# Kernel tuning notes

Hardware: AMD Instinct MI355X
Metric: run time of the kernel (lower is better)

The kernel has to match this reference:

```python
import jax, jax.numpy as jnp
import numpy as np

E = 1024  # embed_dim
NH = 16   # num_heads
HH, WW = 128, 128


def setup_inputs() -> dict:
    key = jax.random.key(0)
    ks = jax.random.split(key, 9)
    s = 0.02
    x = jax.random.normal(ks[0], (1, HH, WW, E), dtype=jnp.float32)
    d = {"x": x}
    for i, name in enumerate(["q", "k", "v", "o"]):
        d[f"W{name}"] = jax.random.normal(ks[1 + 2 * i], (E, E), dtype=jnp.float32) * s
        d[f"b{name}"] = jax.random.normal(ks[2 + 2 * i], (E,), dtype=jnp.float32) * s
    return d


def reference(x, Wq, bq, Wk, bk, Wv, bv, Wo, bo):
    B, h, w, e = x.shape
    D = e // NH  # head dim
    # projections + ReLU feature map on q, k (torch Linear: x @ W.T + b)
    q = jnp.maximum(x @ Wq.T + bq, 0.0).reshape(B, h, w, NH, D)
    k = jnp.maximum(x @ Wk.T + bk, 0.0).reshape(B, h, w, NH, D)
    v = (x @ Wv.T + bv).reshape(B, h, w, NH, D)
    # width-axis linear retention: kv state per (row h, head n)
    kv_w = jnp.einsum('bhwnd,bhwne->bhnde', k, v)        # [B,h,NH,D,D]
    out = jnp.einsum('bhwnd,bhnde->bhwne', q, kv_w)      # [B,h,w,NH,D]
    # height-axis linear retention: kv state per (col w, head n)
    kv_h = jnp.einsum('bhwnd,bhwne->bwnde', k, v)        # [B,w,NH,D,D]
    out = jnp.einsum('bhwne,bwnef->bhwnf', out, kv_h)    # [B,h,w,NH,D]
    out = out.reshape(B, h, w, e) @ Wo.T + bo
    return out.reshape(B, h * w, e)
```

## Files before the change

kernel.cpp:

```cpp
#include <hip/hip_runtime.h>
#include <hip/hip_bf16.h>
#include <stdint.h>


typedef __attribute__((ext_vector_type(4))) float floatx4;
typedef __attribute__((ext_vector_type(8))) short shortx8;

static __device__ __forceinline__ float bf2f(unsigned short h) {
  return __uint_as_float(((unsigned int)h) << 16);
}
static __device__ __forceinline__ unsigned short f2bf(float f) {
  unsigned int u = __float_as_uint(f);
  u += 0x7fffu + ((u >> 16) & 1u);
  return (unsigned short)(u >> 16);
}

static __device__ __forceinline__ void gload16(const void* g, void* l) {
  __builtin_amdgcn_global_load_lds(
      (const __attribute__((address_space(1))) void*)g,
      (__attribute__((address_space(3))) void*)l, 16, 0, 0);
}

__global__ __launch_bounds__(256) void cvt_all(
    const float* __restrict__ x, const float* __restrict__ Wq,
    const float* __restrict__ Wk, const float* __restrict__ Wv,
    const float* __restrict__ Wo, unsigned short* __restrict__ xb,
    unsigned short* __restrict__ wqkvb, unsigned short* __restrict__ wob) {
  const int b = blockIdx.x;
  const float* src;
  unsigned short* dst;
  int off;
  if (b < 16384) {
    src = x; dst = xb; off = b;
  } else if (b < 17408) {
    src = Wq; dst = wqkvb; off = b - 16384;
  } else if (b < 18432) {
    src = Wk; dst = wqkvb + 1048576; off = b - 17408;
  } else if (b < 19456) {
    src = Wv; dst = wqkvb + 2097152; off = b - 18432;
  } else {
    src = Wo; dst = wob; off = b - 19456;
  }
  const int i = (off * 256 + threadIdx.x) * 4;
  float4 f = *(const float4*)(src + i);
  ushort4 o;
  o.x = f2bf(f.x); o.y = f2bf(f.y); o.z = f2bf(f.z); o.w = f2bf(f.w);
  *(ushort4*)(dst + i) = o;
}

template <int MODE>
__global__ __launch_bounds__(256) void gemm_bt(
    const unsigned short* __restrict__ A,
    const unsigned short* __restrict__ BT,
    const float* __restrict__ b0, const float* __restrict__ b1,
    const float* __restrict__ b2,
    unsigned short* __restrict__ Oq, unsigned short* __restrict__ Ok,
    unsigned short* __restrict__ Ov, float* __restrict__ Of) {
  __shared__ __align__(16) unsigned short smem[18432];
  unsigned short* lA = smem;
  unsigned short* lB = smem + 4096;
  const int K = 1024;
  const int t = threadIdx.x;
  const int m0 = blockIdx.x * 128;
  const int n0 = blockIdx.y * 128;
  const int lane = t & 63;
  const int wv = t >> 6;
  const int wm = (wv & 1) * 64;
  const int wn = (wv >> 1) * 64;
  const int mrow = lane & 15;
  const int quad = lane >> 4;
  const int slot = quad ^ ((mrow >> 1) & 3);

  const int srow = t >> 2;
  const int scol = (((t & 3) ^ ((srow >> 1) & 3))) * 8;
  const unsigned short* gA0 = A + (size_t)(m0 + srow) * K + scol;
  const unsigned short* gA1 = A + (size_t)(m0 + 64 + srow) * K + scol;
  const unsigned short* gB0 = BT + (size_t)(n0 + srow) * K + scol;
  const unsigned short* gB1 = BT + (size_t)(n0 + 64 + srow) * K + scol;
  unsigned short* lA0 = &lA[t * 8];
  unsigned short* lA1 = &lA[2048 + t * 8];
  unsigned short* lB0 = &lB[t * 8];
  unsigned short* lB1 = &lB[2048 + t * 8];

  floatx4 acc[4][4] = {};
  for (int kk = 0; kk < K; kk += 32) {
    gload16(gA0 + kk, lA0);
    gload16(gA1 + kk, lA1);
    gload16(gB0 + kk, lB0);
    gload16(gB1 + kk, lB1);
    __syncthreads();
    shortx8 af[4], bfr[4];
#pragma unroll
    for (int i = 0; i < 4; ++i)
      af[i] = *(const shortx8*)&lA[(wm + i * 16 + mrow) * 32 + slot * 8];
#pragma unroll
    for (int j = 0; j < 4; ++j)
      bfr[j] = *(const shortx8*)&lB[(wn + j * 16 + mrow) * 32 + slot * 8];
#pragma unroll
    for (int i = 0; i < 4; ++i)
#pragma unroll
      for (int j = 0; j < 4; ++j)
        acc[i][j] = __builtin_amdgcn_mfma_f32_16x16x32_bf16(af[i], bfr[j],
                                                            acc[i][j], 0, 0, 0);
    __syncthreads();
  }

  if (MODE == 0) {
    const int sel = n0 >> 10;
    const float* bb = (sel == 0) ? b0 : ((sel == 1) ? b1 : b2);
    unsigned short* O = (sel == 0) ? Oq : ((sel == 1) ? Ok : Ov);
    const int nb = n0 & 1023;
    unsigned short* we = smem + wv * 4608;
#pragma unroll
    for (int j = 0; j < 4; ++j) {
      const int coll = j * 16 + mrow;
      const float bias = bb[nb + wn + coll];
#pragma unroll
      for (int i = 0; i < 4; ++i) {
#pragma unroll
        for (int r = 0; r < 4; ++r) {
          const int rowl = i * 16 + quad * 4 + r;
          float v = acc[i][j][r] + bias;
          if (sel < 2) v = fmaxf(v, 0.0f);
          we[rowl * 72 + coll] = f2bf(v);
        }
      }
    }
    __syncthreads();
    const int r8 = lane >> 3;
    const int c8 = lane & 7;
#pragma unroll
    for (int p = 0; p < 8; ++p) {
      const int rowl = r8 + p * 8;
      uint4 v = *(const uint4*)&we[rowl * 72 + c8 * 8];
      *(uint4*)&O[(size_t)(m0 + wm + rowl) * 1024 + nb + wn + c8 * 8] = v;
    }
  } else {
    float* wef = (float*)smem;
    float* we = wef + (wv & 1) * (64 * 68);
    const int r8 = lane >> 3;
    const int c8 = lane & 7;
#pragma unroll
    for (int round = 0; round < 2; ++round) {
      if ((wv >> 1) == round) {
#pragma unroll
        for (int j = 0; j < 4; ++j) {
          const int coll = j * 16 + mrow;
          const float bias = b0[n0 + wn + coll];
#pragma unroll
          for (int i = 0; i < 4; ++i) {
#pragma unroll
            for (int r = 0; r < 4; ++r)
              we[(i * 16 + quad * 4 + r) * 68 + coll] = acc[i][j][r] + bias;
          }
        }
      }
      __syncthreads();
      if ((wv >> 1) == round) {
#pragma unroll
        for (int p = 0; p < 8; ++p) {
          const int rowl = r8 + p * 8;
          float4 v0 = *(const float4*)&we[rowl * 68 + c8 * 8];
          float4 v1 = *(const float4*)&we[rowl * 68 + c8 * 8 + 4];
          float* dst = Of + (size_t)(m0 + wm + rowl) * 1024 + n0 + wn + c8 * 8;
          *(float4*)dst = v0;
          *(float4*)(dst + 4) = v1;
        }
      }
      __syncthreads();
    }
  }
}

__global__ __launch_bounds__(256) void retention_fused(
    const unsigned short* __restrict__ S, const unsigned short* __restrict__ Kb,
    const unsigned short* __restrict__ Vb, unsigned short* __restrict__ D,
    int axis) {
  const int outer = blockIdx.x;
  const int n = blockIdx.y;
  __shared__ unsigned short lS[128 * 72];
  __shared__ unsigned short lKT[64 * 136];
  __shared__ unsigned short lVT[64 * 136];
  unsigned short* lKV = lVT;
  const int t = threadIdx.x;
  const size_t base = (axis == 0) ? ((size_t)outer << 17) : ((size_t)outer << 10);
  const size_t istr = (axis == 0) ? (size_t)1024 : (size_t)131072;
  const size_t nof = (size_t)(n << 6);

#pragma unroll
  for (int it = 0; it < 4; ++it) {
    const int r = it * 32 + (t >> 3);
    const int c = (t & 7) * 8;
    uint4 v = *(const uint4*)&S[base + (size_t)r * istr + nof + c];
    *(uint4*)&lS[r * 72 + c] = v;
  }
#pragma unroll
  for (int it = 0; it < 4; ++it) {
    const int w = it * 32 + (t & 31);
    const int d0 = (t >> 5) * 8;
    const size_t g = base + (size_t)w * istr + nof + d0;
    uint4 k4 = *(const uint4*)&Kb[g];
    uint4 v4 = *(const uint4*)&Vb[g];
    const unsigned short* kp = (const unsigned short*)&k4;
    const unsigned short* vp = (const unsigned short*)&v4;
#pragma unroll
    for (int i = 0; i < 8; ++i) {
      lKT[(d0 + i) * 136 + w] = kp[i];
      lVT[(d0 + i) * 136 + w] = vp[i];
    }
  }
  __syncthreads();

  const int lane = t & 63;
  const int wv = t >> 6;
  const int mrow = lane & 15;
  const int quad = lane >> 4;

  floatx4 acc1[4] = {};
#pragma unroll
  for (int ks = 0; ks < 4; ++ks) {
    shortx8 a = *(const shortx8*)&lVT[(wv * 16 + mrow) * 136 + ks * 32 + quad * 8];
#pragma unroll
    for (int j = 0; j < 4; ++j) {
      shortx8 b = *(const shortx8*)&lKT[(j * 16 + mrow) * 136 + ks * 32 + quad * 8];
      acc1[j] = __builtin_amdgcn_mfma_f32_16x16x32_bf16(a, b, acc1[j], 0, 0, 0);
    }
  }
  __syncthreads();
#pragma unroll
  for (int j = 0; j < 4; ++j)
#pragma unroll
    for (int r = 0; r < 4; ++r)
      lKV[(wv * 16 + quad * 4 + r) * 72 + j * 16 + mrow] = f2bf(acc1[j][r]);
  __syncthreads();

  floatx4 acc2[2][4] = {};
#pragma unroll
  for (int ks = 0; ks < 2; ++ks) {
    shortx8 a2[2], b2[4];
#pragma unroll
    for (int i = 0; i < 2; ++i)
      a2[i] = *(const shortx8*)&lS[(wv * 32 + i * 16 + mrow) * 72 + ks * 32 + quad * 8];
#pragma unroll
    for (int j = 0; j < 4; ++j)
      b2[j] = *(const shortx8*)&lKV[(j * 16 + mrow) * 72 + ks * 32 + quad * 8];
#pragma unroll
    for (int i = 0; i < 2; ++i)
#pragma unroll
      for (int j = 0; j < 4; ++j)
        acc2[i][j] = __builtin_amdgcn_mfma_f32_16x16x32_bf16(a2[i], b2[j],
                                                             acc2[i][j], 0, 0, 0);
  }
  __syncthreads();
#pragma unroll
  for (int i = 0; i < 2; ++i)
#pragma unroll
    for (int j = 0; j < 4; ++j)
#pragma unroll
      for (int r = 0; r < 4; ++r) {
        const int row = wv * 32 + i * 16 + quad * 4 + r;
        const int col = j * 16 + mrow;
        lS[row * 72 + col] = f2bf(acc2[i][j][r]);
      }
  __syncthreads();
#pragma unroll
  for (int it = 0; it < 4; ++it) {
    const int row = it * 32 + (t >> 3);
    const int c = (t & 7) * 8;
    uint4 v = *(const uint4*)&lS[row * 72 + c];
    *(uint4*)&D[base + (size_t)row * istr + nof + c] = v;
  }
}

extern "C" void kernel_launch(void* const* d_in, const int* in_sizes, int n_in,
                              void* d_out, int out_size, void* d_ws, size_t ws_size,
                              hipStream_t stream) {
  const float* x  = (const float*)d_in[0];
  const float* Wq = (const float*)d_in[1];
  const float* bq = (const float*)d_in[2];
  const float* Wk = (const float*)d_in[3];
  const float* bk = (const float*)d_in[4];
  const float* Wv = (const float*)d_in[5];
  const float* bv = (const float*)d_in[6];
  const float* Wo = (const float*)d_in[7];
  const float* bo = (const float*)d_in[8];
  float* out = (float*)d_out;

  char* ws = (char*)d_ws;
  unsigned short* xb    = (unsigned short*)(ws + 0);
  unsigned short* wqkvb = (unsigned short*)(ws + 33554432);
  unsigned short* wob   = (unsigned short*)(ws + 39845888);
  unsigned short* qb    = (unsigned short*)(ws + 41943040);
  unsigned short* kb    = (unsigned short*)(ws + 75497472);
  unsigned short* vb    = (unsigned short*)(ws + 109051904);
  unsigned short* out1  = xb;
  unsigned short* out2  = qb;

  cvt_all<<<dim3(20480), dim3(256), 0, stream>>>(x, Wq, Wk, Wv, Wo, xb, wqkvb, wob);
  gemm_bt<0><<<dim3(128, 24), dim3(256), 0, stream>>>(
      xb, wqkvb, bq, bk, bv, qb, kb, vb, (float*)nullptr);
  retention_fused<<<dim3(128, 16), dim3(256), 0, stream>>>(qb, kb, vb, out1, 0);
  retention_fused<<<dim3(128, 16), dim3(256), 0, stream>>>(out1, kb, vb, out2, 1);
  gemm_bt<1><<<dim3(128, 8), dim3(256), 0, stream>>>(
      out2, wob, bo, nullptr, nullptr, nullptr, nullptr, nullptr, out);
}
```

Before: 350.6 us.

## Replace 128x128 GEMM with double-buffered 256x256 tile, 8-wave pipelined kernel

The QKV and output projection GEMMs now use 256x256 tiles with 512 threads, K-step 64, and double-buffered LDS staging. Global-to-LDS loads for the next tiles are interleaved between MFMA quarter-blocks using explicit vmcnt waits, barriers and setprio. Block IDs are remapped so neighbouring blocks share A/B rows in cache, and the epilogue uses an XOR-swizzled LDS layout. The aim is to hide memory latency and raise data reuse per tile. In exchange the kernel uses 128KB of LDS and more registers, and the grid gets smaller (768 and 256 blocks).

```diff
diff --git a/kernel.cpp b/kernel.cpp
--- a/kernel.cpp
+++ b/kernel.cpp
@@ -6,9 +6,6 @@
 typedef __attribute__((ext_vector_type(4))) float floatx4;
 typedef __attribute__((ext_vector_type(8))) short shortx8;
 
-static __device__ __forceinline__ float bf2f(unsigned short h) {
-  return __uint_as_float(((unsigned int)h) << 16);
-}
 static __device__ __forceinline__ unsigned short f2bf(float f) {
   unsigned int u = __float_as_uint(f);
   u += 0x7fffu + ((u >> 16) & 1u);
@@ -48,61 +45,142 @@
   *(ushort4*)(dst + i) = o;
 }
 
+#define BARRIER()                           \
+  do {                                      \
+    asm volatile("" ::: "memory");          \
+    __builtin_amdgcn_s_barrier();           \
+    asm volatile("" ::: "memory");          \
+  } while (0)
+#define LGKM0 asm volatile("s_waitcnt lgkmcnt(0)" ::: "memory")
+#define VMCNT(N) asm volatile("s_waitcnt vmcnt(" #N ")" ::: "memory")
+
 template <int MODE>
-__global__ __launch_bounds__(256) void gemm_bt(
+__global__ __launch_bounds__(512, 2) void gemm256(
     const unsigned short* __restrict__ A,
     const unsigned short* __restrict__ BT,
     const float* __restrict__ b0, const float* __restrict__ b1,
     const float* __restrict__ b2,
     unsigned short* __restrict__ Oq, unsigned short* __restrict__ Ok,
     unsigned short* __restrict__ Ov, float* __restrict__ Of) {
-  __shared__ __align__(16) unsigned short smem[18432];
-  unsigned short* lA = smem;
-  unsigned short* lB = smem + 4096;
-  const int K = 1024;
+  __shared__ __align__(16) unsigned short smem[65536];
   const int t = threadIdx.x;
-  const int m0 = blockIdx.x * 128;
-  const int n0 = blockIdx.y * 128;
-  const int lane = t & 63;
-  const int wv = t >> 6;
-  const int wm = (wv & 1) * 64;
-  const int wn = (wv >> 1) * 64;
-  const int mrow = lane & 15;
-  const int quad = lane >> 4;
-  const int slot = quad ^ ((mrow >> 1) & 3);
-
-  const int srow = t >> 2;
-  const int scol = (((t & 3) ^ ((srow >> 1) & 3))) * 8;
-  const unsigned short* gA0 = A + (size_t)(m0 + srow) * K + scol;
-  const unsigned short* gA1 = A + (size_t)(m0 + 64 + srow) * K + scol;
-  const unsigned short* gB0 = BT + (size_t)(n0 + srow) * K + scol;
-  const unsigned short* gB1 = BT + (size_t)(n0 + 64 + srow) * K + scol;
-  unsigned short* lA0 = &lA[t * 8];
-  unsigned short* lA1 = &lA[2048 + t * 8];
-  unsigned short* lB0 = &lB[t * 8];
-  unsigned short* lB1 = &lB[2048 + t * 8];
-
-  floatx4 acc[4][4] = {};
-  for (int kk = 0; kk < K; kk += 32) {
-    gload16(gA0 + kk, lA0);
-    gload16(gA1 + kk, lA1);
-    gload16(gB0 + kk, lB0);
-    gload16(gB1 + kk, lB1);
-    __syncthreads();
-    shortx8 af[4], bfr[4];
-#pragma unroll
-    for (int i = 0; i < 4; ++i)
-      af[i] = *(const shortx8*)&lA[(wm + i * 16 + mrow) * 32 + slot * 8];
-#pragma unroll
-    for (int j = 0; j < 4; ++j)
-      bfr[j] = *(const shortx8*)&lB[(wn + j * 16 + mrow) * 32 + slot * 8];
-#pragma unroll
-    for (int i = 0; i < 4; ++i)
-#pragma unroll
-      for (int j = 0; j < 4; ++j)
-        acc[i][j] = __builtin_amdgcn_mfma_f32_16x16x32_bf16(af[i], bfr[j],
-                                                            acc[i][j], 0, 0, 0);
-    __syncthreads();
+  const int lane = t & 63, wid = t >> 6;
+  const int wm = wid >> 2, wn = wid & 3;
+  const int mrow = lane & 15, quad = lane >> 4;
+
+  int bid = blockIdx.x, bm, bn;
+  if (MODE == 0) {
+    int s = (bid & 7) * 96 + (bid >> 3);
+    bm = s / 12; bn = s - bm * 12;
+  } else {
+    int s = (bid & 7) * 32 + (bid >> 3);
+    bm = s >> 2; bn = s & 3;
+  }
+  const int m0 = bm << 8;
+  const int n0 = bn << 8;
+
+  const int sw0 = ((quad ^ (mrow & 7)) << 3);
+  const int sw1 = (((quad ^ 4) ^ (mrow & 7)) << 3);
+  const int a_base = wm * 8192 + mrow * 64;
+  const int b_base = 16384 + (wn >> 1) * 8192 + (((wn & 1) << 6) + mrow) * 64;
+  const int s_dst0 = wid * 512 + lane * 8;
+  const int srow = wid * 8 + (lane >> 3);
+  const int csrc = ((lane & 7) ^ (lane >> 3)) << 3;
+  const unsigned short* gAbase = A + (size_t)(m0 + srow) * 1024 + csrc;
+  const unsigned short* gBbase = BT + (size_t)(n0 + srow) * 1024 + csrc;
+
+#define STAGE_A(KT, H)                                              \
+  do {                                                              \
+    const unsigned short* _g = gAbase + ((H) << 17) + ((KT) << 6);  \
+    const int _d = (((KT) & 1) << 15) + ((H) << 13) + s_dst0;       \
+    gload16(_g, &smem[_d]);                                         \
+    gload16(_g + 65536, &smem[_d + 4096]);                          \
+  } while (0)
+#define STAGE_B(KT, H)                                                     \
+  do {                                                                     \
+    const unsigned short* _g = gBbase + ((H) << 17) + ((KT) << 6);         \
+    const int _d = (((KT) & 1) << 15) + 16384 + ((H) << 13) + s_dst0;      \
+    gload16(_g, &smem[_d]);                                                \
+    gload16(_g + 65536, &smem[_d + 4096]);                                 \
+  } while (0)
+#define LDA(MH)                                                  \
+  do {                                                           \
+    const int _ab = cb + a_base + ((MH) << 12);                  \
+    _Pragma("unroll") for (int i = 0; i < 4; ++i) {              \
+      aF[i][0] = *(const shortx8*)&smem[_ab + i * 1024 + sw0];   \
+      aF[i][1] = *(const shortx8*)&smem[_ab + i * 1024 + sw1];   \
+    }                                                            \
+  } while (0)
+#define LDB(NH)                                                      \
+  do {                                                               \
+    const int _bb = cb + b_base + ((NH) << 11);                      \
+    _Pragma("unroll") for (int j = 0; j < 2; ++j) {                  \
+      bF[NH][j][0] = *(const shortx8*)&smem[_bb + j * 1024 + sw0];   \
+      bF[NH][j][1] = *(const shortx8*)&smem[_bb + j * 1024 + sw1];   \
+    }                                                                \
+  } while (0)
+#define MFMAQ(MH, NH)                                                        \
+  do {                                                                       \
+    _Pragma("unroll") for (int ks = 0; ks < 2; ++ks)                         \
+    _Pragma("unroll") for (int i = 0; i < 4; ++i)                            \
+    _Pragma("unroll") for (int j = 0; j < 2; ++j)                            \
+      acc[(MH) * 4 + i][(NH) * 2 + j] =                                      \
+          __builtin_amdgcn_mfma_f32_16x16x32_bf16(                           \
+              aF[i][ks], bF[NH][j][ks], acc[(MH) * 4 + i][(NH) * 2 + j], 0,  \
+              0, 0);                                                         \
+  } while (0)
+
+  floatx4 acc[8][4] = {};
+  shortx8 aF[4][2];
+  shortx8 bF[2][2][2];
+
+  STAGE_A(0, 0); STAGE_A(0, 1);
+  STAGE_B(0, 0); STAGE_B(0, 1);
+  STAGE_B(1, 0); STAGE_B(1, 1);
+  VMCNT(4);
+  BARRIER();
+
+#pragma unroll 2
+  for (int kt = 0; kt < 16; ++kt) {
+    const int cb = (kt & 1) << 15;
+    LDA(0);
+    LDB(0);
+    if (kt < 15) STAGE_A(kt + 1, 0);
+    BARRIER();
+    LGKM0;
+    __builtin_amdgcn_sched_barrier(0);
+    __builtin_amdgcn_s_setprio(1);
+    MFMAQ(0, 0);
+    __builtin_amdgcn_s_setprio(0);
+    BARRIER();
+    LDB(1);
+    if (kt < 15) STAGE_A(kt + 1, 1);
+    BARRIER();
+    LGKM0;
+    __builtin_amdgcn_sched_barrier(0);
+    __builtin_amdgcn_s_setprio(1);
+    MFMAQ(0, 1);
+    __builtin_amdgcn_s_setprio(0);
+    BARRIER();
+    LDA(1);
+    if (kt < 14) STAGE_B(kt + 2, 0);
+    BARRIER();
+    LGKM0;
+    __builtin_amdgcn_sched_barrier(0);
+    __builtin_amdgcn_s_setprio(1);
+    MFMAQ(1, 1);
+    __builtin_amdgcn_s_setprio(0);
+    BARRIER();
+    if (kt < 14) STAGE_B(kt + 2, 1);
+    __builtin_amdgcn_s_setprio(1);
+    MFMAQ(1, 0);
+    __builtin_amdgcn_s_setprio(0);
+    if (kt < 14) {
+      VMCNT(4);
+    } else {
+      VMCNT(0);
+    }
+    BARRIER();
   }
 
   if (MODE == 0) {
@@ -110,66 +188,66 @@
     const float* bb = (sel == 0) ? b0 : ((sel == 1) ? b1 : b2);
     unsigned short* O = (sel == 0) ? Oq : ((sel == 1) ? Ok : Ov);
     const int nb = n0 & 1023;
-    unsigned short* we = smem + wv * 4608;
-#pragma unroll
-    for (int j = 0; j < 4; ++j) {
-      const int coll = j * 16 + mrow;
-      const float bias = bb[nb + wn + coll];
-#pragma unroll
-      for (int i = 0; i < 4; ++i) {
+    float bias[4];
+#pragma unroll
+    for (int j = 0; j < 4; ++j) bias[j] = bb[nb + wn * 64 + j * 16 + mrow];
+    unsigned short* we = &smem[wid * 8192];
+#pragma unroll
+    for (int mr = 0; mr < 8; ++mr)
+#pragma unroll
+      for (int j = 0; j < 4; ++j)
 #pragma unroll
         for (int r = 0; r < 4; ++r) {
-          const int rowl = i * 16 + quad * 4 + r;
-          float v = acc[i][j][r] + bias;
+          const int row = mr * 16 + quad * 4 + r;
+          const int col = j * 16 + mrow;
+          float v = acc[mr][j][r] + bias[j];
           if (sel < 2) v = fmaxf(v, 0.0f);
-          we[rowl * 72 + coll] = f2bf(v);
+          we[row * 64 + (((col >> 3) ^ (row & 7)) << 3) + (col & 7)] = f2bf(v);
         }
-      }
-    }
     __syncthreads();
-    const int r8 = lane >> 3;
-    const int c8 = lane & 7;
-#pragma unroll
-    for (int p = 0; p < 8; ++p) {
-      const int rowl = r8 + p * 8;
-      uint4 v = *(const uint4*)&we[rowl * 72 + c8 * 8];
-      *(uint4*)&O[(size_t)(m0 + wm + rowl) * 1024 + nb + wn + c8 * 8] = v;
+#pragma unroll
+    for (int it = 0; it < 16; ++it) {
+      const int rr = it * 8 + (lane >> 3);
+      const int cl = lane & 7;
+      uint4 v = *(const uint4*)&we[rr * 64 + ((cl ^ (rr & 7)) << 3)];
+      *(uint4*)&O[(size_t)(m0 + wm * 128 + rr) * 1024 + nb + wn * 64 + cl * 8] =
+          v;
     }
   } else {
-    float* wef = (float*)smem;
-    float* we = wef + (wv & 1) * (64 * 68);
-    const int r8 = lane >> 3;
-    const int c8 = lane & 7;
-#pragma unroll
-    for (int round = 0; round < 2; ++round) {
-      if ((wv >> 1) == round) {
-#pragma unroll
-        for (int j = 0; j < 4; ++j) {
-          const int coll = j * 16 + mrow;
-          const float bias = b0[n0 + wn + coll];
-#pragma unroll
-          for (int i = 0; i < 4; ++i) {
-#pragma unroll
-            for (int r = 0; r < 4; ++r)
-              we[(i * 16 + quad * 4 + r) * 68 + coll] = acc[i][j][r] + bias;
+    float* wef = (float*)&smem[wid * 8192];
+    float bias[4];
+#pragma unroll
+    for (int j = 0; j < 4; ++j) bias[j] = b0[n0 + wn * 64 + j * 16 + mrow];
+#pragma unroll
+    for (int h = 0; h < 2; ++h) {
+#pragma unroll
+      for (int i = 0; i < 4; ++i)
+#pragma unroll
+        for (int j = 0; j < 4; ++j)
+#pragma unroll
+          for (int r = 0; r < 4; ++r) {
+            const int row = i * 16 + quad * 4 + r;
+            const int col = j * 16 + mrow;
+            wef[row * 64 + (((col >> 2) ^ (row & 7)) << 2) + (col & 3)] =
+                acc[h * 4 + i][j][r] + bias[j];
           }
-        }
+      __syncthreads();
+#pragma unroll
+      for (int it = 0; it < 16; ++it) {
+        const int rr = it * 4 + (lane >> 4);
+        const int cl = lane & 15;
+        float4 v = *(const float4*)&wef[rr * 64 + ((cl ^ (rr & 7)) << 2)];
+        *(float4*)&Of[(size_t)(m0 + wm * 128 + h * 64 + rr) * 1024 + n0 +
+                      wn * 64 + cl * 4] = v;
       }
       __syncthreads();
-      if ((wv >> 1) == round) {
-#pragma unroll
-        for (int p = 0; p < 8; ++p) {
-          const int rowl = r8 + p * 8;
-          float4 v0 = *(const float4*)&we[rowl * 68 + c8 * 8];
-          float4 v1 = *(const float4*)&we[rowl * 68 + c8 * 8 + 4];
-          float* dst = Of + (size_t)(m0 + wm + rowl) * 1024 + n0 + wn + c8 * 8;
-          *(float4*)dst = v0;
-          *(float4*)(dst + 4) = v1;
-        }
-      }
-      __syncthreads();
-    }
-  }
+    }
+  }
+#undef STAGE_A
+#undef STAGE_B
+#undef LDA
+#undef LDB
+#undef MFMAQ
 }
 
 __global__ __launch_bounds__(256) void retention_fused(
@@ -297,10 +375,10 @@
   unsigned short* out2  = qb;
 
   cvt_all<<<dim3(20480), dim3(256), 0, stream>>>(x, Wq, Wk, Wv, Wo, xb, wqkvb, wob);
-  gemm_bt<0><<<dim3(128, 24), dim3(256), 0, stream>>>(
+  gemm256<0><<<dim3(768), dim3(512), 0, stream>>>(
       xb, wqkvb, bq, bk, bv, qb, kb, vb, (float*)nullptr);
   retention_fused<<<dim3(128, 16), dim3(256), 0, stream>>>(qb, kb, vb, out1, 0);
   retention_fused<<<dim3(128, 16), dim3(256), 0, stream>>>(out1, kb, vb, out2, 1);
-  gemm_bt<1><<<dim3(128, 8), dim3(256), 0, stream>>>(
+  gemm256<1><<<dim3(256), dim3(512), 0, stream>>>(
       out2, wob, bo, nullptr, nullptr, nullptr, nullptr, nullptr, out);
 }
```

After: 328.5 us. 6.3% less time.
